# Performance work log

Hardware: AMD Instinct MI355X
Metric: run time of the kernel (lower is better)

## Reference

```python
import jax, jax.numpy as jnp
import numpy as np

EPS = 1e-5

def layer_norm(x, gamma, beta):
    # biased variance (unbiased=False), matching torch code
    mean = jnp.mean(x, axis=-1, keepdims=True)
    var = jnp.mean((x - mean) ** 2, axis=-1, keepdims=True)
    return (x - mean) / jnp.sqrt(var + EPS) * gamma + beta

def setup_inputs() -> dict:
    key = jax.random.key(0)
    ks = jax.random.split(key, 8)
    B, T, C, H = 2, 2048, 768, 12
    Dff = 4 * C
    s = lambda n: 1.0 / np.sqrt(n)
    return {
        "x": jax.random.normal(ks[0], (B, T, C), dtype=jnp.float32),
        "mask": jnp.ones((B, T), dtype=jnp.int32),
        "Wqkv": jax.random.normal(ks[1], (C, 3 * C), dtype=jnp.float32) * s(C),
        "bqkv": jnp.zeros((3 * C,), dtype=jnp.float32),
        "Wp": jax.random.normal(ks[2], (C, C), dtype=jnp.float32) * s(C),
        "bp": jnp.zeros((C,), dtype=jnp.float32),
        "gamma1": jnp.ones((1, 1, C), dtype=jnp.float32),
        "beta1": jnp.zeros((1, 1, C), dtype=jnp.float32),
        "W1": jax.random.normal(ks[3], (C, Dff), dtype=jnp.float32) * s(C),
        "b1": jnp.zeros((Dff,), dtype=jnp.float32),
        "W2": jax.random.normal(ks[4], (Dff, C), dtype=jnp.float32) * s(Dff),
        "b2": jnp.zeros((C,), dtype=jnp.float32),
        "gamma2": jnp.ones((1, 1, C), dtype=jnp.float32),
        "beta2": jnp.zeros((1, 1, C), dtype=jnp.float32),
    }

def reference(x, mask, Wqkv, bqkv, Wp, bp, gamma1, beta1, W1, b1, W2, b2, gamma2, beta2):
    B, T, C = x.shape
    H = 12
    D = C // H
    # --- multi-head attention (hand-rolled QK^T-softmax-V) ---
    qkv = x @ Wqkv + bqkv                                  # (B,T,3C)
    q, k, v = jnp.split(qkv, 3, axis=-1)
    q = q.reshape(B, T, H, D).transpose(0, 2, 1, 3)        # (B,H,T,D)
    k = k.reshape(B, T, H, D).transpose(0, 2, 1, 3)
    v = v.reshape(B, T, H, D).transpose(0, 2, 1, 3)
    scores = jnp.einsum('bhtd,bhsd->bhts', q, k) * (D ** -0.5)  # (B,H,T,T)
    pad = (mask == 0)[:, None, None, :]                    # (B,1,1,T)
    scores = jnp.where(pad, -jnp.inf, scores)
    weights = jax.nn.softmax(scores, axis=-1)
    attn = jnp.einsum('bhts,bhsd->bhtd', weights, v)       # (B,H,T,D)
    attn = attn.transpose(0, 2, 1, 3).reshape(B, T, C)
    attn = attn @ Wp + bp
    # --- post-sublayer LN then residual (as in source) ---
    out = x + layer_norm(attn, gamma1, beta1)
    # --- MLP with exact GELU ---
    h = jax.nn.gelu(out @ W1 + b1, approximate=False)
    mlp = h @ W2 + b2
    out = out + layer_norm(mlp, gamma2, beta2)
    return out
```

## Files before the change

kernel.cpp:

```cpp
#include <hip/hip_runtime.h>
#include <math.h>

#define BB 2
#define TT 2048
#define CC 768
#define NH 12
#define HD 64
#define DFF 3072
#define MM (BB*TT)

typedef _Float16 f16;
typedef unsigned long long u64;
typedef unsigned int u32;
typedef __attribute__((ext_vector_type(8))) _Float16 f16x8;
typedef __attribute__((ext_vector_type(4))) _Float16 f16x4;
typedef __attribute__((ext_vector_type(4))) float f32x4;

#define QSCALE 0.18033688011112042f

#define GLD_LDS(gptr, lptr) \
  __builtin_amdgcn_global_load_lds((const __attribute__((address_space(1))) void*)(gptr), \
                                   (__attribute__((address_space(3))) void*)(lptr), 16, 0, 0)

#if __has_builtin(__builtin_amdgcn_exp2f)
#define EXP2(x) __builtin_amdgcn_exp2f(x)
#else
#define EXP2(x) exp2f(x)
#endif

#if __has_builtin(__builtin_amdgcn_rcpf)
#define RCP(x) __builtin_amdgcn_rcpf(x)
#else
#define RCP(x) (1.f / (x))
#endif

__device__ __forceinline__ float gelu_f(float x)
{
    const float y = fabsf(x) * 0.70710678118654752f;
    const float t = RCP(fmaf(0.3275911f, y, 1.f));
    float p = fmaf(1.061405429f, t, -1.453152027f);
    p = fmaf(p, t, 1.421413741f);
    p = fmaf(p, t, -0.284496736f);
    p = fmaf(p, t, 0.254829592f);
    p = p * t;
    const float e = EXP2(-y * y * 1.4426950408889634f);
    const float er = copysignf(1.f - p * e, x);
    return 0.5f * x * (1.f + er);
}

__global__ __launch_bounds__(256)
void convert_f16(const float* __restrict__ in, f16* __restrict__ out, int n4)
{
    const int i = blockIdx.x * 256 + threadIdx.x;
    if (i >= n4) return;
    float4 v = ((const float4*)in)[i];
    f16x4 o = {(f16)v.x, (f16)v.y, (f16)v.z, (f16)v.w};
    ((f16x4*)out)[i] = o;
}

__global__ __launch_bounds__(256)
void convert_transpose(const float* __restrict__ W, f16* __restrict__ Wt,
                       int K, int N)
{
    __shared__ float tile[32][33];
    const int k0 = blockIdx.x * 32, n0 = blockIdx.y * 32;
    const int r  = threadIdx.x >> 3;
    const int c4 = (threadIdx.x & 7) * 4;
    float4 v = *(const float4*)&W[(size_t)(k0 + r) * N + n0 + c4];
    tile[r][c4 + 0] = v.x; tile[r][c4 + 1] = v.y;
    tile[r][c4 + 2] = v.z; tile[r][c4 + 3] = v.w;
    __syncthreads();
    f16x4 o = {(f16)tile[c4 + 0][r], (f16)tile[c4 + 1][r],
               (f16)tile[c4 + 2][r], (f16)tile[c4 + 3][r]};
    *(f16x4*)&Wt[(size_t)(n0 + r) * K + k0 + c4] = o;
}

template<int TM, int OUT_MODE, int GELU, int SPLITK>
__global__ __launch_bounds__(256)
void gemm_mfma(const f16* __restrict__ A, const f16* __restrict__ Bt,
               const float* __restrict__ bias, void* __restrict__ Cout,
               f16* __restrict__ Kout, f16* __restrict__ Vout,
               const int* __restrict__ maskp, int M, int N, int K)
{
    constexpr int NT = (TM == 128) ? 4 : 2;
    constexpr int G  = 512 / TM;
    __shared__ f16 As[2][TM * 32];
    __shared__ f16 Bs[2][128 * 32];

    int id = blockIdx.x;
    int kk = 0;
    if (SPLITK == 2) { kk = id & 1; id >>= 1; }
    const int xcd = id & 7, j = id >> 3;
    const int by = xcd * G + (j & (G - 1));
    const int bx = j / G;
    const int Keff = K / SPLITK;

    const int t = threadIdx.x;
    const int lane = t & 63, w = t >> 6;
    const int fr = lane & 15, quad = lane >> 4;
    const int row0 = by * TM, col0 = bx * 128;
    const int wm = (TM == 128) ? (w & 1) * 64 : 0;
    const int wn = (TM == 128) ? (w >> 1) * 64 : w * 32;

    const int arow = w * (TM / 4) + (lane >> 2);
    const int brow = w * 32 + (lane >> 2);
    const int cg = (((lane & 3) ^ ((lane >> 3) & 3)) * 16);
    const char* ag = (const char*)(A  + (size_t)(row0 + arow) * K + kk * Keff) + cg;
    const char* bg = (const char*)(Bt + (size_t)(col0 + brow) * K + kk * Keff) + cg;
    const size_t rowK = (size_t)K * 2;
    const int wA = w * (TM / 4) * 32;
    const int wB = w * 32 * 32;
    const int sof = (quad ^ ((fr >> 1) & 3)) * 8;

    f32x4 acc[4][NT] = {};

    GLD_LDS(ag, &As[0][wA]);
    if (TM == 128) GLD_LDS(ag + 16 * rowK, &As[0][wA + 16 * 32]);
    GLD_LDS(bg, &Bs[0][wB]);
    GLD_LDS(bg + 16 * rowK, &Bs[0][wB + 16 * 32]);

    for (int k0 = 0; k0 < Keff; k0 += 32) {
        const int buf = (k0 >> 5) & 1;
        __syncthreads();
        if (k0 + 32 < Keff) {
            const size_t kb = (size_t)(k0 + 32) * 2;
            GLD_LDS(ag + kb, &As[buf ^ 1][wA]);
            if (TM == 128) GLD_LDS(ag + kb + 16 * rowK, &As[buf ^ 1][wA + 16 * 32]);
            GLD_LDS(bg + kb, &Bs[buf ^ 1][wB]);
            GLD_LDS(bg + kb + 16 * rowK, &Bs[buf ^ 1][wB + 16 * 32]);
        }
        f16x8 af[4], bf[NT];
#pragma unroll
        for (int mt = 0; mt < 4; ++mt)
            af[mt] = *(const f16x8*)&As[buf][(wm + mt * 16 + fr) * 32 + sof];
#pragma unroll
        for (int nt = 0; nt < NT; ++nt)
            bf[nt] = *(const f16x8*)&Bs[buf][(wn + nt * 16 + fr) * 32 + sof];
#pragma unroll
        for (int mt = 0; mt < 4; ++mt)
#pragma unroll
            for (int nt = 0; nt < NT; ++nt)
                acc[mt][nt] = __builtin_amdgcn_mfma_f32_16x16x32_f16(
                    af[mt], bf[nt], acc[mt][nt], 0, 0, 0);
    }

    float bvs[NT];
#pragma unroll
    for (int nt = 0; nt < NT; ++nt)
        bvs[nt] = (SPLITK == 2 && kk) ? 0.f : bias[col0 + wn + nt * 16 + fr];
    f16* outbase = (f16*)Cout + (SPLITK == 2 ? (size_t)kk * M * N : 0);
#pragma unroll
    for (int mt = 0; mt < 4; ++mt) {
        const int rowb = row0 + wm + mt * 16 + quad * 4;
        float mv[4] = {1.f, 1.f, 1.f, 1.f};
        if (OUT_MODE == 2 && col0 >= 1536) {
            int4 mi = *(const int4*)&maskp[rowb];
            mv[0] = mi.x ? 1.f : 0.f; mv[1] = mi.y ? 1.f : 0.f;
            mv[2] = mi.z ? 1.f : 0.f; mv[3] = mi.w ? 1.f : 0.f;
        }
#pragma unroll
        for (int nt = 0; nt < NT; ++nt) {
            const int col = col0 + wn + nt * 16 + fr;
            if (OUT_MODE == 2) {
                const int bq = rowb >> 11, sb = rowb & 2047;
                if (col0 < 768) {
#pragma unroll
                    for (int v = 0; v < 4; ++v)
                        ((f16*)Cout)[(size_t)(rowb + v) * 768 + col]
                            = (f16)((acc[mt][nt][v] + bvs[nt]) * QSCALE);
                } else if (col0 < 1536) {
                    const int dg = col - 768;
                    const int hh = dg >> 6, dd = dg & 63;
                    f16* kb = Kout + (size_t)(bq * NH + hh) * (TT * HD);
#pragma unroll
                    for (int v = 0; v < 4; ++v) {
                        const int s = sb + v;
                        kb[((s >> 4) * 128 + (dd >> 3) * 16 + (s & 15)) * 8 + (dd & 7)]
                            = (f16)(acc[mt][nt][v] + bvs[nt]);
                    }
                } else {
                    const int dg = col - 1536;
                    const int hh = dg >> 6, dd = dg & 63;
                    f16* vb = Vout + (size_t)(bq * NH + hh) * (TT * HD);
                    f16x4 pk = {(f16)((acc[mt][nt][0] + bvs[nt]) * mv[0]),
                                (f16)((acc[mt][nt][1] + bvs[nt]) * mv[1]),
                                (f16)((acc[mt][nt][2] + bvs[nt]) * mv[2]),
                                (f16)((acc[mt][nt][3] + bvs[nt]) * mv[3])};
                    *(f16x4*)&vb[((sb >> 3) * 64 + dd) * 8 + (sb & 7)] = pk;
                }
            } else {
#pragma unroll
                for (int v = 0; v < 4; ++v) {
                    float o = acc[mt][nt][v] + bvs[nt];
                    if (GELU) o = gelu_f(o);
                    outbase[(size_t)(rowb + v) * N + col] = (f16)o;
                }
            }
        }
    }
}

__global__ __launch_bounds__(256)
void attn_mfma(const f16* __restrict__ qh, const f16* __restrict__ kth,
               const f16* __restrict__ vth, const int* __restrict__ mask,
               f16* __restrict__ out)
{
    __shared__ __align__(16) char smem[16640];
    f16* Mf = (f16*)smem;
    f16* Ps = (f16*)(smem + 4096);
    float* Ored  = (float*)smem;
    float* lredp = (float*)(smem + 16384);

    const int id = blockIdx.x;
    const int xcd = id & 7, j = id >> 3;
    const int pair = xcd * 3 + j % 3;
    const int qt = j / 3;
    const int b = pair / NH, h = pair % NH;

    const int t = threadIdx.x, lane = t & 63, w = t >> 6;
    const int wq = w >> 1, ws = w & 1;
    const int fr = lane & 15, quad = lane >> 4;

    {
        int4 mi0 = *(const int4*)&mask[b * TT + t * 8];
        int4 mi1 = *(const int4*)&mask[b * TT + t * 8 + 4];
        f16x8 mrow;
        mrow[0] = mi0.x ? (f16)1.f : (f16)0.f; mrow[1] = mi0.y ? (f16)1.f : (f16)0.f;
        mrow[2] = mi0.z ? (f16)1.f : (f16)0.f; mrow[3] = mi0.w ? (f16)1.f : (f16)0.f;
        mrow[4] = mi1.x ? (f16)1.f : (f16)0.f; mrow[5] = mi1.y ? (f16)1.f : (f16)0.f;
        mrow[6] = mi1.z ? (f16)1.f : (f16)0.f; mrow[7] = mi1.w ? (f16)1.f : (f16)0.f;
        *(f16x8*)&Mf[t * 8] = mrow;
    }

    f16x8 qf[2][2];
#pragma unroll
    for (int nt = 0; nt < 2; ++nt)
#pragma unroll
        for (int ks = 0; ks < 2; ++ks)
            qf[nt][ks] = *(const f16x8*)&qh[(size_t)(b * TT + qt * 64 + wq * 32 + nt * 16 + fr) * CC
                                            + h * HD + ks * 32 + quad * 8];

    __syncthreads();

    const f16* KB = kth + (size_t)(b * NH + h) * (TT * HD);
    const f16* VB = vth + (size_t)(b * NH + h) * (TT * HD);
    int ko[2][2], vo[4];
#pragma unroll
    for (int mt = 0; mt < 2; ++mt)
#pragma unroll
        for (int ks = 0; ks < 2; ++ks)
            ko[mt][ks] = ((ws * 2 + mt) * 128 + (ks * 4 + quad) * 16 + fr) * 8;
#pragma unroll
    for (int nt = 0; nt < 4; ++nt)
        vo[nt] = ((ws * 4 + quad) * 64 + nt * 16 + fr) * 8;

    f32x4 oacc[2][4] = {};
    f32x4 lacc[2] = {};

#pragma unroll 2
    for (int it = 0; it < TT / 64; ++it) {
        const int ib = it * 4096;
        f16x8 vf[4];
#pragma unroll
        for (int nt = 0; nt < 4; ++nt)
            vf[nt] = *(const f16x8*)(VB + ib + vo[nt]);
        f16x8 kf[2][2];
#pragma unroll
        for (int mt = 0; mt < 2; ++mt)
#pragma unroll
            for (int ks = 0; ks < 2; ++ks)
                kf[mt][ks] = *(const f16x8*)(KB + ib + ko[mt][ks]);

        f32x4 sacc[2][2] = {};
#pragma unroll
        for (int mt = 0; mt < 2; ++mt)
#pragma unroll
            for (int nt = 0; nt < 2; ++nt) {
                sacc[mt][nt] = __builtin_amdgcn_mfma_f32_16x16x32_f16(
                    kf[mt][0], qf[nt][0], sacc[mt][nt], 0, 0, 0);
                sacc[mt][nt] = __builtin_amdgcn_mfma_f32_16x16x32_f16(
                    kf[mt][1], qf[nt][1], sacc[mt][nt], 0, 0, 0);
            }

#pragma unroll
        for (int mt = 0; mt < 2; ++mt)
#pragma unroll
            for (int nt = 0; nt < 2; ++nt) {
                f16x4 pk = {(f16)EXP2(sacc[mt][nt][0]), (f16)EXP2(sacc[mt][nt][1]),
                            (f16)EXP2(sacc[mt][nt][2]), (f16)EXP2(sacc[mt][nt][3])};
                *(f16x4*)&Ps[(wq * 32 + nt * 16 + fr) * 72 + ws * 32 + mt * 16 + quad * 4] = pk;
            }

        f16x8 mf = *(const f16x8*)&Mf[it * 64 + ws * 32 + quad * 8];
        f16x8 pf[2];
#pragma unroll
        for (int mt = 0; mt < 2; ++mt)
            pf[mt] = *(const f16x8*)&Ps[(wq * 32 + mt * 16 + fr) * 72 + ws * 32 + quad * 8];
#pragma unroll
        for (int mt = 0; mt < 2; ++mt) {
            lacc[mt] = __builtin_amdgcn_mfma_f32_16x16x32_f16(pf[mt], mf, lacc[mt], 0, 0, 0);
#pragma unroll
            for (int nt = 0; nt < 4; ++nt)
                oacc[mt][nt] = __builtin_amdgcn_mfma_f32_16x16x32_f16(
                    pf[mt], vf[nt], oacc[mt][nt], 0, 0, 0);
        }
    }

    __syncthreads();
    if (ws == 1) {
#pragma unroll
        for (int mt = 0; mt < 2; ++mt) {
            const int q = wq * 32 + mt * 16 + quad * 4;
#pragma unroll
            for (int nt = 0; nt < 4; ++nt)
#pragma unroll
                for (int v = 0; v < 4; ++v)
                    Ored[(q + v) * 64 + nt * 16 + fr] = oacc[mt][nt][v];
            if (fr == 0)
#pragma unroll
                for (int v = 0; v < 4; ++v) lredp[q + v] = lacc[mt][v];
        }
    }
    __syncthreads();
    if (ws == 0) {
#pragma unroll
        for (int mt = 0; mt < 2; ++mt) {
            const int q0 = wq * 32 + mt * 16 + quad * 4;
            float linv[4];
#pragma unroll
            for (int v = 0; v < 4; ++v)
                linv[v] = 1.f / (lacc[mt][v] + lredp[q0 + v]);
#pragma unroll
            for (int nt = 0; nt < 4; ++nt)
#pragma unroll
                for (int v = 0; v < 4; ++v) {
                    float o = oacc[mt][nt][v] + Ored[(q0 + v) * 64 + nt * 16 + fr];
                    out[(size_t)(b * TT + qt * 64 + q0 + v) * CC + h * HD + nt * 16 + fr]
                        = (f16)(o * linv[v]);
                }
        }
    }
}

template<int WRITE_H>
__global__ __launch_bounds__(256)
void ln_residual(const float* __restrict__ res,
                 const f16* __restrict__ y0, const f16* __restrict__ y1,
                 const float* __restrict__ gamma, const float* __restrict__ beta,
                 float* __restrict__ outp, f16* __restrict__ outh)
{
    const int t = threadIdx.x;
    const int row = blockIdx.x * 8 + (t >> 5);
    const int c0 = (t & 31) * 24;
    const f16* yr0 = y0 + (size_t)row * CC + c0;
    const f16* yr1 = y1 + (size_t)row * CC + c0;
    float v[24];
    float s = 0.f, sq = 0.f;
#pragma unroll
    for (int i = 0; i < 3; ++i) {
        f16x8 a = *(const f16x8*)(yr0 + i * 8);
        f16x8 bb = *(const f16x8*)(yr1 + i * 8);
#pragma unroll
        for (int jj = 0; jj < 8; ++jj) {
            float vv = (float)a[jj] + (float)bb[jj];
            v[i * 8 + jj] = vv; s += vv; sq += vv * vv;
        }
    }
#pragma unroll
    for (int off = 1; off < 32; off <<= 1) {
        s  += __shfl_xor(s, off);
        sq += __shfl_xor(sq, off);
    }
    const float mean = s * (1.f / 768.f);
    const float var  = sq * (1.f / 768.f) - mean * mean;
    const float rstd = rsqrtf(var + 1e-5f);
    const float* rr = res + (size_t)row * CC + c0;
    float* orow = outp + (size_t)row * CC + c0;
#pragma unroll
    for (int i = 0; i < 6; ++i) {
        float4 r4 = *(const float4*)(rr + i * 4);
        float4 g4 = *(const float4*)(gamma + c0 + i * 4);
        float4 b4 = *(const float4*)(beta + c0 + i * 4);
        float4 o;
        o.x = r4.x + (v[i*4+0] - mean) * rstd * g4.x + b4.x;
        o.y = r4.y + (v[i*4+1] - mean) * rstd * g4.y + b4.y;
        o.z = r4.z + (v[i*4+2] - mean) * rstd * g4.z + b4.z;
        o.w = r4.w + (v[i*4+3] - mean) * rstd * g4.w + b4.w;
        *(float4*)(orow + i * 4) = o;
        if (WRITE_H) {
            f16x4 h4 = {(f16)o.x, (f16)o.y, (f16)o.z, (f16)o.w};
            *(f16x4*)(outh + (size_t)row * CC + c0 + i * 4) = h4;
        }
    }
}

extern "C" void kernel_launch(void* const* d_in, const int* in_sizes, int n_in,
                              void* d_out, int out_size, void* d_ws, size_t ws_size,
                              hipStream_t stream)
{
    const float* x     = (const float*)d_in[0];
    const int*   mask  = (const int*)  d_in[1];
    const float* Wqkv  = (const float*)d_in[2];
    const float* bqkv  = (const float*)d_in[3];
    const float* Wp    = (const float*)d_in[4];
    const float* bp    = (const float*)d_in[5];
    const float* g1    = (const float*)d_in[6];
    const float* be1   = (const float*)d_in[7];
    const float* W1    = (const float*)d_in[8];
    const float* b1    = (const float*)d_in[9];
    const float* W2    = (const float*)d_in[10];
    const float* b2    = (const float*)d_in[11];
    const float* g2    = (const float*)d_in[12];
    const float* be2   = (const float*)d_in[13];
    float* outp = (float*)d_out;

    char* wsb = (char*)d_ws;
    f16*   qhb    = (f16*)(wsb);
    f16*   kth    = (f16*)(wsb + 6291456);
    f16*   vth    = (f16*)(wsb + 12582912);
    f16*   attnh  = (f16*)(wsb + 18874368);
    f16*   hbuf   = (f16*)(wsb);
    f16*   xh     = (f16*)(wsb + 25165824);
    float* out1f  = (float*)(wsb + 25165824);
    f16*   Wqkvt  = (f16*)(wsb + 31457280);
    f16*   Wpt    = (f16*)(wsb + 34996224);
    f16*   W1t    = (f16*)(wsb + 37748736);
    f16*   W2t    = (f16*)(wsb + 42467328);
    f16*   p0     = (f16*)(wsb + 47185920);
    f16*   p1     = (f16*)(wsb + 53477376);
    f16*   out1h  = (f16*)(wsb + 59768832);

    const dim3 blk(256);

    convert_f16<<<dim3(MM * CC / 1024), blk, 0, stream>>>(x, xh, MM * CC / 4);
    convert_transpose<<<dim3(CC / 32, 3 * CC / 32), blk, 0, stream>>>(Wqkv, Wqkvt, CC, 3 * CC);
    convert_transpose<<<dim3(CC / 32, CC / 32), blk, 0, stream>>>(Wp, Wpt, CC, CC);
    convert_transpose<<<dim3(CC / 32, DFF / 32), blk, 0, stream>>>(W1, W1t, CC, DFF);
    convert_transpose<<<dim3(DFF / 32, CC / 32), blk, 0, stream>>>(W2, W2t, DFF, CC);

    gemm_mfma<128, 2, 0, 1><<<dim3((3 * CC / 128) * (MM / 128)), blk, 0, stream>>>(
        xh, Wqkvt, bqkv, qhb, kth, vth, mask, MM, 3 * CC, CC);
    attn_mfma<<<dim3((TT / 64) * NH * BB), blk, 0, stream>>>(qhb, kth, vth, mask, attnh);
    gemm_mfma<64, 1, 0, 2><<<dim3(2 * (CC / 128) * (MM / 64)), blk, 0, stream>>>(
        attnh, Wpt, bp, p0, nullptr, nullptr, nullptr, MM, CC, CC);
    ln_residual<1><<<dim3(MM / 8), blk, 0, stream>>>(x, p0, p1, g1, be1, out1f, out1h);
    gemm_mfma<128, 1, 1, 1><<<dim3((DFF / 128) * (MM / 128)), blk, 0, stream>>>(
        out1h, W1t, b1, hbuf, nullptr, nullptr, nullptr, MM, DFF, CC);
    gemm_mfma<64, 1, 0, 2><<<dim3(2 * (CC / 128) * (MM / 64)), blk, 0, stream>>>(
        hbuf, W2t, b2, p0, nullptr, nullptr, nullptr, MM, CC, DFF);
    ln_residual<0><<<dim3(MM / 8), blk, 0, stream>>>(out1f, p0, p1, g2, be2, outp, nullptr);
}
```

Baseline: 277.4 us.

## Split attention over key halves and merge partials inside projection GEMM

Attention now runs twice as many blocks, each covering half the key sequence, and writes unnormalized partial outputs plus row sums. The output-projection GEMM loads both partials, adds them, divides by the combined sum, and stages the result in LDS through registers instead of using direct global-to-LDS loads. The goal is more parallelism in attention, which had only 768 blocks. The cost is extra partial-output traffic and a slower A-load path in the projection GEMM. Separately, the five conversion and transpose kernels are merged into one launch. The split-key merge skips max rescaling, which is only valid if the attention kernel uses a fixed softmax offset and not a per-half running max.

New measurement: 272.6 us. About the same (-1.7%).

```diff
diff --git a/kernel.cpp b/kernel.cpp
--- a/kernel.cpp
+++ b/kernel.cpp
@@ -48,22 +48,13 @@
     return 0.5f * x * (1.f + er);
 }
 
-__global__ __launch_bounds__(256)
-void convert_f16(const float* __restrict__ in, f16* __restrict__ out, int n4)
-{
-    const int i = blockIdx.x * 256 + threadIdx.x;
-    if (i >= n4) return;
-    float4 v = ((const float4*)in)[i];
-    f16x4 o = {(f16)v.x, (f16)v.y, (f16)v.z, (f16)v.w};
-    ((f16x4*)out)[i] = o;
-}
-
-__global__ __launch_bounds__(256)
-void convert_transpose(const float* __restrict__ W, f16* __restrict__ Wt,
-                       int K, int N)
-{
-    __shared__ float tile[32][33];
-    const int k0 = blockIdx.x * 32, n0 = blockIdx.y * 32;
+__device__ __forceinline__ void transpose_tile(const float* __restrict__ W,
+                                               f16* __restrict__ Wt,
+                                               int K, int N, int idx,
+                                               float tile[32][33])
+{
+    const int kx = idx % (K / 32), ny = idx / (K / 32);
+    const int k0 = kx * 32, n0 = ny * 32;
     const int r  = threadIdx.x >> 3;
     const int c4 = (threadIdx.x & 7) * 4;
     float4 v = *(const float4*)&W[(size_t)(k0 + r) * N + n0 + c4];
@@ -75,12 +66,39 @@
     *(f16x4*)&Wt[(size_t)(n0 + r) * K + k0 + c4] = o;
 }
 
-template<int TM, int OUT_MODE, int GELU, int SPLITK>
+__global__ __launch_bounds__(256)
+void conv_all(const float* __restrict__ x, f16* __restrict__ xh,
+              const float* __restrict__ Wqkv, f16* __restrict__ Wqkvt,
+              const float* __restrict__ Wp, f16* __restrict__ Wpt,
+              const float* __restrict__ W1, f16* __restrict__ W1t,
+              const float* __restrict__ W2, f16* __restrict__ W2t)
+{
+    __shared__ float tile[32][33];
+    const int blk = blockIdx.x;
+    if (blk < 3072) {
+        const int i = blk * 256 + threadIdx.x;
+        float4 v = ((const float4*)x)[i];
+        f16x4 o = {(f16)v.x, (f16)v.y, (f16)v.z, (f16)v.w};
+        ((f16x4*)xh)[i] = o;
+    } else if (blk < 4800) {
+        transpose_tile(Wqkv, Wqkvt, CC, 3 * CC, blk - 3072, tile);
+    } else if (blk < 5376) {
+        transpose_tile(Wp, Wpt, CC, CC, blk - 4800, tile);
+    } else if (blk < 7680) {
+        transpose_tile(W1, W1t, CC, DFF, blk - 5376, tile);
+    } else {
+        transpose_tile(W2, W2t, DFF, CC, blk - 7680, tile);
+    }
+}
+
+template<int TM, int OUT_MODE, int GELU, int SPLITK, int AMODE>
 __global__ __launch_bounds__(256)
 void gemm_mfma(const f16* __restrict__ A, const f16* __restrict__ Bt,
                const float* __restrict__ bias, void* __restrict__ Cout,
                f16* __restrict__ Kout, f16* __restrict__ Vout,
-               const int* __restrict__ maskp, int M, int N, int K)
+               const int* __restrict__ maskp, int M, int N, int K,
+               const f16* __restrict__ Ao1,
+               const float* __restrict__ lp0, const float* __restrict__ lp1)
 {
     constexpr int NT = (TM == 128) ? 4 : 2;
     constexpr int G  = 512 / TM;
@@ -112,20 +130,62 @@
     const int wB = w * 32 * 32;
     const int sof = (quad ^ ((fr >> 1) & 3)) * 8;
 
+    const f16 *a0p = nullptr, *a1p = nullptr;
+    const float *lr0 = nullptr, *lr1 = nullptr;
+    int lchunk8 = 0;
+    f16* aswb[2] = {nullptr, nullptr};
+    if (AMODE) {
+        const int strow = lane >> 2, pchunk = lane & 3;
+        lchunk8 = ((pchunk ^ ((lane >> 3) & 3))) * 8;
+        const int ar = row0 + w * 16 + strow;
+        a0p = A   + (size_t)ar * K + kk * Keff + lchunk8;
+        a1p = Ao1 + (size_t)ar * K + kk * Keff + lchunk8;
+        lr0 = lp0 + ar * NH;
+        lr1 = lp1 + ar * NH;
+        aswb[0] = &As[0][wA + strow * 32 + pchunk * 8];
+        aswb[1] = &As[1][wA + strow * 32 + pchunk * 8];
+    }
+
     f32x4 acc[4][NT] = {};
 
-    GLD_LDS(ag, &As[0][wA]);
-    if (TM == 128) GLD_LDS(ag + 16 * rowK, &As[0][wA + 16 * 32]);
+    if (AMODE) {
+        f16x8 a0 = *(const f16x8*)(a0p);
+        f16x8 a1 = *(const f16x8*)(a1p);
+        const int hh = (kk * Keff + lchunk8) >> 6;
+        const f16 lh = (f16)RCP(lr0[hh] + lr1[hh]);
+        f16x8 s;
+#pragma unroll
+        for (int jj = 0; jj < 8; ++jj) s[jj] = (f16)((a0[jj] + a1[jj]) * lh);
+        *(f16x8*)aswb[0] = s;
+    } else {
+        GLD_LDS(ag, &As[0][wA]);
+        if (TM == 128) GLD_LDS(ag + 16 * rowK, &As[0][wA + 16 * 32]);
+    }
     GLD_LDS(bg, &Bs[0][wB]);
     GLD_LDS(bg + 16 * rowK, &Bs[0][wB + 16 * 32]);
 
     for (int k0 = 0; k0 < Keff; k0 += 32) {
         const int buf = (k0 >> 5) & 1;
+        f16x8 na0, na1; float nls = 1.f;
+        if (AMODE && k0 + 32 < Keff) {
+            na0 = *(const f16x8*)(a0p + k0 + 32);
+            na1 = *(const f16x8*)(a1p + k0 + 32);
+            const int hh = (kk * Keff + k0 + 32 + lchunk8) >> 6;
+            nls = lr0[hh] + lr1[hh];
+        }
         __syncthreads();
         if (k0 + 32 < Keff) {
             const size_t kb = (size_t)(k0 + 32) * 2;
-            GLD_LDS(ag + kb, &As[buf ^ 1][wA]);
-            if (TM == 128) GLD_LDS(ag + kb + 16 * rowK, &As[buf ^ 1][wA + 16 * 32]);
+            if (AMODE) {
+                const f16 lh = (f16)RCP(nls);
+                f16x8 s;
+#pragma unroll
+                for (int jj = 0; jj < 8; ++jj) s[jj] = (f16)((na0[jj] + na1[jj]) * lh);
+                *(f16x8*)aswb[buf ^ 1] = s;
+            } else {
+                GLD_LDS(ag + kb, &As[buf ^ 1][wA]);
+                if (TM == 128) GLD_LDS(ag + kb + 16 * rowK, &As[buf ^ 1][wA + 16 * 32]);
+            }
             GLD_LDS(bg + kb, &Bs[buf ^ 1][wB]);
             GLD_LDS(bg + kb + 16 * rowK, &Bs[buf ^ 1][wB + 16 * 32]);
         }
@@ -203,7 +263,8 @@
 __global__ __launch_bounds__(256)
 void attn_mfma(const f16* __restrict__ qh, const f16* __restrict__ kth,
                const f16* __restrict__ vth, const int* __restrict__ mask,
-               f16* __restrict__ out)
+               f16* __restrict__ O0, f16* __restrict__ O1,
+               float* __restrict__ l0, float* __restrict__ l1)
 {
     __shared__ __align__(16) char smem[16640];
     f16* Mf = (f16*)smem;
@@ -214,7 +275,8 @@
     const int id = blockIdx.x;
     const int xcd = id & 7, j = id >> 3;
     const int pair = xcd * 3 + j % 3;
-    const int qt = j / 3;
+    const int rem = j / 3;
+    const int qt = rem >> 1, shalf = rem & 1;
     const int b = pair / NH, h = pair % NH;
 
     const int t = threadIdx.x, lane = t & 63, w = t >> 6;
@@ -257,8 +319,9 @@
     f32x4 oacc[2][4] = {};
     f32x4 lacc[2] = {};
 
+    const int it0 = shalf * 16;
 #pragma unroll 2
-    for (int it = 0; it < TT / 64; ++it) {
+    for (int it = it0; it < it0 + 16; ++it) {
         const int ib = it * 4096;
         f16x8 vf[4];
 #pragma unroll
@@ -306,6 +369,8 @@
         }
     }
 
+    f16* Oout = shalf ? O1 : O0;
+    float* lout = shalf ? l1 : l0;
     __syncthreads();
     if (ws == 1) {
 #pragma unroll
@@ -326,17 +391,18 @@
 #pragma unroll
         for (int mt = 0; mt < 2; ++mt) {
             const int q0 = wq * 32 + mt * 16 + quad * 4;
-            float linv[4];
-#pragma unroll
-            for (int v = 0; v < 4; ++v)
-                linv[v] = 1.f / (lacc[mt][v] + lredp[q0 + v]);
+            if (fr == 0)
+#pragma unroll
+                for (int v = 0; v < 4; ++v)
+                    lout[(size_t)(b * TT + qt * 64 + q0 + v) * NH + h]
+                        = lacc[mt][v] + lredp[q0 + v];
 #pragma unroll
             for (int nt = 0; nt < 4; ++nt)
 #pragma unroll
                 for (int v = 0; v < 4; ++v) {
                     float o = oacc[mt][nt][v] + Ored[(q0 + v) * 64 + nt * 16 + fr];
-                    out[(size_t)(b * TT + qt * 64 + q0 + v) * CC + h * HD + nt * 16 + fr]
-                        = (f16)(o * linv[v]);
+                    Oout[(size_t)(b * TT + qt * 64 + q0 + v) * CC + h * HD + nt * 16 + fr]
+                        = (f16)o;
                 }
         }
     }
@@ -418,7 +484,8 @@
     f16*   qhb    = (f16*)(wsb);
     f16*   kth    = (f16*)(wsb + 6291456);
     f16*   vth    = (f16*)(wsb + 12582912);
-    f16*   attnh  = (f16*)(wsb + 18874368);
+    f16*   O0     = (f16*)(wsb + 18874368);
+    f16*   O1     = (f16*)(wsb + 25165824);
     f16*   hbuf   = (f16*)(wsb);
     f16*   xh     = (f16*)(wsb + 25165824);
     float* out1f  = (float*)(wsb + 25165824);
@@ -429,24 +496,28 @@
     f16*   p0     = (f16*)(wsb + 47185920);
     f16*   p1     = (f16*)(wsb + 53477376);
     f16*   out1h  = (f16*)(wsb + 59768832);
+    float* l0     = (float*)(wsb + 66060288);
+    float* l1     = (float*)(wsb + 66256896);
 
     const dim3 blk(256);
 
-    convert_f16<<<dim3(MM * CC / 1024), blk, 0, stream>>>(x, xh, MM * CC / 4);
-    convert_transpose<<<dim3(CC / 32, 3 * CC / 32), blk, 0, stream>>>(Wqkv, Wqkvt, CC, 3 * CC);
-    convert_transpose<<<dim3(CC / 32, CC / 32), blk, 0, stream>>>(Wp, Wpt, CC, CC);
-    convert_transpose<<<dim3(CC / 32, DFF / 32), blk, 0, stream>>>(W1, W1t, CC, DFF);
-    convert_transpose<<<dim3(DFF / 32, CC / 32), blk, 0, stream>>>(W2, W2t, DFF, CC);
-
-    gemm_mfma<128, 2, 0, 1><<<dim3((3 * CC / 128) * (MM / 128)), blk, 0, stream>>>(
-        xh, Wqkvt, bqkv, qhb, kth, vth, mask, MM, 3 * CC, CC);
-    attn_mfma<<<dim3((TT / 64) * NH * BB), blk, 0, stream>>>(qhb, kth, vth, mask, attnh);
-    gemm_mfma<64, 1, 0, 2><<<dim3(2 * (CC / 128) * (MM / 64)), blk, 0, stream>>>(
-        attnh, Wpt, bp, p0, nullptr, nullptr, nullptr, MM, CC, CC);
+    conv_all<<<dim3(9984), blk, 0, stream>>>(x, xh, Wqkv, Wqkvt, Wp, Wpt,
+                                             W1, W1t, W2, W2t);
+
+    gemm_mfma<128, 2, 0, 1, 0><<<dim3((3 * CC / 128) * (MM / 128)), blk, 0, stream>>>(
+        xh, Wqkvt, bqkv, qhb, kth, vth, mask, MM, 3 * CC, CC,
+        nullptr, nullptr, nullptr);
+    attn_mfma<<<dim3((TT / 64) * NH * BB * 2), blk, 0, stream>>>(
+        qhb, kth, vth, mask, O0, O1, l0, l1);
+    gemm_mfma<64, 1, 0, 2, 1><<<dim3(2 * (CC / 128) * (MM / 64)), blk, 0, stream>>>(
+        O0, Wpt, bp, p0, nullptr, nullptr, nullptr, MM, CC, CC,
+        O1, l0, l1);
     ln_residual<1><<<dim3(MM / 8), blk, 0, stream>>>(x, p0, p1, g1, be1, out1f, out1h);
-    gemm_mfma<128, 1, 1, 1><<<dim3((DFF / 128) * (MM / 128)), blk, 0, stream>>>(
-        out1h, W1t, b1, hbuf, nullptr, nullptr, nullptr, MM, DFF, CC);
-    gemm_mfma<64, 1, 0, 2><<<dim3(2 * (CC / 128) * (MM / 64)), blk, 0, stream>>>(
-        hbuf, W2t, b2, p0, nullptr, nullptr, nullptr, MM, CC, DFF);
+    gemm_mfma<128, 1, 1, 1, 0><<<dim3((DFF / 128) * (MM / 128)), blk, 0, stream>>>(
+        out1h, W1t, b1, hbuf, nullptr, nullptr, nullptr, MM, DFF, CC,
+        nullptr, nullptr, nullptr);
+    gemm_mfma<64, 1, 0, 2, 0><<<dim3(2 * (CC / 128) * (MM / 64)), blk, 0, stream>>>(
+        hbuf, W2t, b2, p0, nullptr, nullptr, nullptr, MM, CC, DFF,
+        nullptr, nullptr, nullptr);
     ln_residual<0><<<dim3(MM / 8), blk, 0, stream>>>(out1f, p0, p1, g2, be2, outp, nullptr);
 }
```
